# Performance work log

Measured on AMD Instinct MI355X. Metric: run time of the kernel, lower is better.

## Reference

```python
import jax, jax.numpy as jnp
import numpy as np

HEADS = 8
DIM_HEAD = 64
SCALE = DIM_HEAD ** -0.5
THRESH = 0.01


def setup_inputs() -> dict:
    key = jax.random.key(0)
    ks = jax.random.split(key, 5)
    b, n, dim = 4, 2048, 512
    inner = HEADS * DIM_HEAD  # 512
    x = jax.random.normal(ks[0], (b, n, dim), dtype=jnp.float32)
    Wqkv = jax.random.normal(ks[1], (dim, 3 * inner), dtype=jnp.float32) * (dim ** -0.5)
    bqkv = jax.random.normal(ks[2], (3 * inner,), dtype=jnp.float32) * 0.02
    Wout = jax.random.normal(ks[3], (inner, dim), dtype=jnp.float32) * (inner ** -0.5)
    bout = jax.random.normal(ks[4], (dim,), dtype=jnp.float32) * 0.02
    return {"x": x, "Wqkv": Wqkv, "bqkv": bqkv, "Wout": Wout, "bout": bout}


def reference(x, Wqkv, bqkv, Wout, bout):
    b, n, dim = x.shape
    qkv = x @ Wqkv + bqkv  # [b, n, 3*inner]
    q, k, v = jnp.split(qkv, 3, axis=-1)
    # b n (h d) -> b h n d
    split_heads = lambda t: t.reshape(b, n, HEADS, DIM_HEAD).transpose(0, 2, 1, 3)
    q, k, v = split_heads(q), split_heads(k), split_heads(v)
    dots = jnp.einsum('bhid,bhjd->bhij', q, k) * SCALE
    attn = jax.nn.softmax(dots, axis=-1)
    attn = jnp.where(attn > THRESH, attn, jnp.zeros_like(attn))
    out = jnp.einsum('bhij,bhjd->bhid', attn, v)
    out = out.transpose(0, 2, 1, 3).reshape(b, n, HEADS * DIM_HEAD)
    return out @ Wout + bout
```

## Files before the change

### kernel.cpp

```cpp
#include <hip/hip_runtime.h>

#define S_   2048
#define DM   512
#define HD   64
#define BHN  32

typedef unsigned short u16;
typedef __bf16 bf16x8 __attribute__((ext_vector_type(8)));
typedef float  f32x4  __attribute__((ext_vector_type(4)));

__device__ __forceinline__ float bf2f(u16 u) {
    union { unsigned int i; float f; } v; v.i = ((unsigned int)u) << 16; return v.f;
}
__device__ __forceinline__ u16 f2bf(float f) {
    union { float f; unsigned int i; } v; v.f = f;
    unsigned int i = v.i;
    return (u16)((i + 0x7FFFu + ((i >> 16) & 1u)) >> 16);
}
__device__ __forceinline__ void split3(float x, u16& b0, u16& b1, u16& b2) {
    b0 = f2bf(x);
    const float r0 = x - bf2f(b0);
    b1 = f2bf(r0);
    const float r1 = r0 - bf2f(b1);
    b2 = f2bf(r1);
}
__device__ __forceinline__ void split3t(float x, u16& b0, u16& b1, u16& b2) {
    union { float f; unsigned int i; } v; v.f = x;
    const unsigned int i0 = v.i & 0xFFFF0000u;
    b0 = (u16)(i0 >> 16);
    union { float f; unsigned int i; } w0c; w0c.i = i0;
    const float r0 = x - w0c.f;
    union { float f; unsigned int i; } u; u.f = r0;
    const unsigned int i1 = u.i & 0xFFFF0000u;
    b1 = (u16)(i1 >> 16);
    union { float f; unsigned int i; } w1c; w1c.i = i1;
    const float r1 = r0 - w1c.f;
    union { float f; unsigned int i; } z; z.f = r1;
    b2 = (u16)(z.i >> 16);
}

__global__ __launch_bounds__(256) void prep_split_wT(
    const float* __restrict__ W, int N, int total,
    u16* __restrict__ w0, u16* __restrict__ w1, u16* __restrict__ w2)
{
    for (int idx = blockIdx.x * 256 + threadIdx.x; idx < total; idx += gridDim.x * 256) {
        const int n = idx >> 9, k = idx & 511;
        u16 a0, a1, a2;
        split3t(W[(size_t)k * N + n], a0, a1, a2);
        w0[idx] = a0; w1[idx] = a1;
        if (w2) w2[idx] = a2;
    }
}

__global__ __launch_bounds__(256) void gemm_qkv_mfma(
    const float* __restrict__ A, const u16* __restrict__ Wt0, const u16* __restrict__ Wt1,
    const u16* __restrict__ Wt2, const float* __restrict__ bias,
    float* __restrict__ qh, float* __restrict__ kh, u16* __restrict__ khi,
    u16* __restrict__ vt)
{
    __shared__ __attribute__((aligned(16))) u16 As0[128 * 32], As1[128 * 32], As2[128 * 32];
    __shared__ __attribute__((aligned(16))) u16 Bs0[128 * 32], Bs1[128 * 32], Bs2[128 * 32];

    const int t  = threadIdx.x;
    const int m0 = blockIdx.y * 128, n0 = blockIdx.x * 128;
    const int w  = t >> 6, l = t & 63;
    const int wm = (w >> 1) * 64, wn = (w & 1) * 64;
    const int lr = l & 15, lq = l >> 4;

    const f32x4 zero4 = {0.f, 0.f, 0.f, 0.f};
    f32x4 acc[4][4];
#pragma unroll
    for (int i = 0; i < 4; i++)
#pragma unroll
        for (int j = 0; j < 4; j++) acc[i][j] = zero4;

    for (int k0 = 0; k0 < 512; k0 += 32) {
        __syncthreads();
#pragma unroll
        for (int i = 0; i < 4; i++) {
            const int e = t + 256 * i;
            const int r = e >> 3, c4 = (e & 7) * 4;
            const float4 f = *(const float4*)(&A[(size_t)(m0 + r) * 512 + k0 + c4]);
            const float xv[4] = {f.x, f.y, f.z, f.w};
            u16 a0[4], a1[4], a2[4];
#pragma unroll
            for (int j = 0; j < 4; j++) split3t(xv[j], a0[j], a1[j], a2[j]);
            int2 p0, p1, p2;
            p0.x = a0[0] | (a0[1] << 16); p0.y = a0[2] | (a0[3] << 16);
            p1.x = a1[0] | (a1[1] << 16); p1.y = a1[2] | (a1[3] << 16);
            p2.x = a2[0] | (a2[1] << 16); p2.y = a2[2] | (a2[3] << 16);
            *(int2*)(&As0[r * 32 + c4]) = p0;
            *(int2*)(&As1[r * 32 + c4]) = p1;
            *(int2*)(&As2[r * 32 + c4]) = p2;
        }
#pragma unroll
        for (int i = 0; i < 2; i++) {
            const int e = t + 256 * i;
            const int r = e >> 2, c0 = (e & 3) * 8;
            *(int4*)(&Bs0[r * 32 + c0]) = *(const int4*)(&Wt0[(size_t)(n0 + r) * 512 + k0 + c0]);
            *(int4*)(&Bs1[r * 32 + c0]) = *(const int4*)(&Wt1[(size_t)(n0 + r) * 512 + k0 + c0]);
            *(int4*)(&Bs2[r * 32 + c0]) = *(const int4*)(&Wt2[(size_t)(n0 + r) * 512 + k0 + c0]);
        }
        __syncthreads();

#pragma unroll
        for (int i = 0; i < 4; i++) {
            const int ao = (wm + i * 16 + lr) * 32 + lq * 8;
            const bf16x8 a0 = *(const bf16x8*)(&As0[ao]);
            const bf16x8 a1 = *(const bf16x8*)(&As1[ao]);
            const bf16x8 a2 = *(const bf16x8*)(&As2[ao]);
#pragma unroll
            for (int j = 0; j < 4; j++) {
                const int bo = (wn + j * 16 + lr) * 32 + lq * 8;
                const bf16x8 b0 = *(const bf16x8*)(&Bs0[bo]);
                const bf16x8 b1 = *(const bf16x8*)(&Bs1[bo]);
                const bf16x8 b2 = *(const bf16x8*)(&Bs2[bo]);
                f32x4 c = acc[i][j];
                c = __builtin_amdgcn_mfma_f32_16x16x32_bf16(a0, b0, c, 0, 0, 0);
                c = __builtin_amdgcn_mfma_f32_16x16x32_bf16(a0, b1, c, 0, 0, 0);
                c = __builtin_amdgcn_mfma_f32_16x16x32_bf16(a1, b0, c, 0, 0, 0);
                c = __builtin_amdgcn_mfma_f32_16x16x32_bf16(a1, b1, c, 0, 0, 0);
                c = __builtin_amdgcn_mfma_f32_16x16x32_bf16(a0, b2, c, 0, 0, 0);
                c = __builtin_amdgcn_mfma_f32_16x16x32_bf16(a2, b0, c, 0, 0, 0);
                acc[i][j] = c;
            }
        }
    }

#pragma unroll
    for (int j = 0; j < 4; j++) {
        const int n = n0 + wn + j * 16 + lr;
        const float bv = bias[n];
        const int part = n >> 9, within = n & 511;
        const int h = within >> 6, d = within & 63;
#pragma unroll
        for (int i = 0; i < 4; i++) {
#pragma unroll
            for (int r = 0; r < 4; r++) {
                const int m = m0 + wm + i * 16 + lq * 4 + r;
                const int b = m >> 11, ns = m & 2047;
                const float val = acc[i][j][r] + bv;
                if (part == 0) {
                    qh[(((size_t)(b * 8 + h)) * S_ + ns) * HD + d] = val;
                } else if (part == 1) {
                    const size_t kidx = (((size_t)(b * 8 + h)) * S_ + ns) * HD + d;
                    kh[kidx]  = val;
                    khi[kidx] = f2bf(val);
                } else {
                    vt[(((size_t)(b * 8 + h)) * HD + d) * S_ + ns] = f2bf(val);
                }
            }
        }
    }
}

__global__ __launch_bounds__(512) void attn_mfma128(
    const float* __restrict__ q_ws, const float* __restrict__ k_ws,
    const u16* __restrict__ khi_ws, const u16* __restrict__ vt_ws,
    u16* __restrict__ ao_ws)
{
    __shared__ __attribute__((aligned(16))) u16 pool[2][3][4096];
    __shared__ float smaxL[8][32];

    const int t  = threadIdx.x;
    const int w  = t >> 6, l = t & 63;
    const int lr = l & 15, lq = l >> 4;
    const int bh = blockIdx.y, b = bh >> 3, h = bh & 7;
    const int q0 = blockIdx.x * 128;

    const float* qg  = q_ws + ((size_t)bh * S_ + q0) * HD;
    const float* kg0 = k_ws + (size_t)bh * S_ * HD;
    const u16*   kh0 = khi_ws + (size_t)bh * S_ * HD;
    const u16*   vb  = vt_ws + (size_t)bh * HD * S_;

    const int cw = t >> 6, cl = t & 63;
    const int sr = ((cw >> 1) << 4) | (cl & 15);
    const int sd = ((cw & 1) << 5) | (((cl >> 4) & 3) << 3);
    const int sdst = t * 8;

    bf16x8 fq0[2], fq1[2], fq2[2];
#pragma unroll
    for (int h2 = 0; h2 < 2; h2++) {
        __syncthreads();
        {
            const float* src = qg + (size_t)h2 * 4096 + sr * 64 + sd;
            const float4 fA = *(const float4*)(src);
            const float4 fB = *(const float4*)(src + 4);
            const float xv[8] = {fA.x * 0.125f, fA.y * 0.125f, fA.z * 0.125f, fA.w * 0.125f,
                                 fB.x * 0.125f, fB.y * 0.125f, fB.z * 0.125f, fB.w * 0.125f};
            u16 a0[8], a1[8], a2[8];
#pragma unroll
            for (int j = 0; j < 8; j++) split3(xv[j], a0[j], a1[j], a2[j]);
            int4 p0, p1, p2;
            p0.x = a0[0] | (a0[1] << 16); p0.y = a0[2] | (a0[3] << 16);
            p0.z = a0[4] | (a0[5] << 16); p0.w = a0[6] | (a0[7] << 16);
            p1.x = a1[0] | (a1[1] << 16); p1.y = a1[2] | (a1[3] << 16);
            p1.z = a1[4] | (a1[5] << 16); p1.w = a1[6] | (a1[7] << 16);
            p2.x = a2[0] | (a2[1] << 16); p2.y = a2[2] | (a2[3] << 16);
            p2.z = a2[4] | (a2[5] << 16); p2.w = a2[6] | (a2[7] << 16);
            *(int4*)(&pool[0][0][sdst]) = p0;
            *(int4*)(&pool[0][1][sdst]) = p1;
            *(int4*)(&pool[0][2][sdst]) = p2;
        }
        __syncthreads();
        if ((w >> 2) == h2) {
#pragma unroll
            for (int kc = 0; kc < 2; kc++) {
                const int o = ((((w & 3) << 1) + kc) << 9) + l * 8;
                fq0[kc] = *(const bf16x8*)(&pool[0][0][o]);
                fq1[kc] = *(const bf16x8*)(&pool[0][1][o]);
                fq2[kc] = *(const bf16x8*)(&pool[0][2][o]);
            }
        }
    }

    const f32x4 zero4 = {0.f, 0.f, 0.f, 0.f};
    float lsum[4];
#pragma unroll
    for (int r = 0; r < 4; r++) lsum[r] = 0.f;

    int cur = 0;
    {
        const float* src = kg0 + sr * 64 + sd;
        const float4 fA = *(const float4*)(src);
        const float4 fB = *(const float4*)(src + 4);
        __syncthreads();
        const float xv[8] = {fA.x, fA.y, fA.z, fA.w, fB.x, fB.y, fB.z, fB.w};
        u16 a0[8], a1[8], a2[8];
#pragma unroll
        for (int j = 0; j < 8; j++) split3t(xv[j], a0[j], a1[j], a2[j]);
        int4 p0, p1, p2;
        p0.x = a0[0] | (a0[1] << 16); p0.y = a0[2] | (a0[3] << 16);
        p0.z = a0[4] | (a0[5] << 16); p0.w = a0[6] | (a0[7] << 16);
        p1.x = a1[0] | (a1[1] << 16); p1.y = a1[2] | (a1[3] << 16);
        p1.z = a1[4] | (a1[5] << 16); p1.w = a1[6] | (a1[7] << 16);
        p2.x = a2[0] | (a2[1] << 16); p2.y = a2[2] | (a2[3] << 16);
        p2.z = a2[4] | (a2[5] << 16); p2.w = a2[6] | (a2[7] << 16);
        *(int4*)(&pool[0][0][sdst]) = p0;
        *(int4*)(&pool[0][1][sdst]) = p1;
        *(int4*)(&pool[0][2][sdst]) = p2;
        __syncthreads();
    }

    for (int jt = 0; jt < 32; jt++) {
        const int jn = (jt + 1 < 32) ? jt + 1 : 31;
        const float* src = kg0 + (size_t)jn * 4096 + sr * 64 + sd;
        const float4 fA = *(const float4*)(src);
        const float4 fB = *(const float4*)(src + 4);

        const u16* K0c = pool[cur][0];
        const u16* K1c = pool[cur][1];
        const u16* K2c = pool[cur][2];
        float tmax = -1e30f;
#pragma unroll
        for (int nt = 0; nt < 4; nt++) {
            f32x4 aHH = zero4, aC = zero4;
#pragma unroll
            for (int kc = 0; kc < 2; kc++) {
                const int ko = (((nt << 1) + kc) << 9) + l * 8;
                const bf16x8 k0 = *(const bf16x8*)(&K0c[ko]);
                const bf16x8 k1 = *(const bf16x8*)(&K1c[ko]);
                const bf16x8 k2 = *(const bf16x8*)(&K2c[ko]);
                aHH = __builtin_amdgcn_mfma_f32_16x16x32_bf16(fq0[kc], k0, aHH, 0, 0, 0);
                aC  = __builtin_amdgcn_mfma_f32_16x16x32_bf16(fq0[kc], k1, aC, 0, 0, 0);
                aC  = __builtin_amdgcn_mfma_f32_16x16x32_bf16(fq1[kc], k0, aC, 0, 0, 0);
                aC  = __builtin_amdgcn_mfma_f32_16x16x32_bf16(fq1[kc], k1, aC, 0, 0, 0);
                aC  = __builtin_amdgcn_mfma_f32_16x16x32_bf16(fq0[kc], k2, aC, 0, 0, 0);
                aC  = __builtin_amdgcn_mfma_f32_16x16x32_bf16(fq2[kc], k0, aC, 0, 0, 0);
            }
#pragma unroll
            for (int r = 0; r < 4; r++) {
                const float s = fminf(fmaxf(aHH[r] + aC[r], -30.f), 30.f);
                tmax = fmaxf(tmax, s);
                lsum[r] += __expf(s);
            }
        }
#pragma unroll
        for (int off = 1; off < 64; off <<= 1)
            tmax = fmaxf(tmax, __shfl_xor(tmax, off, 64));
        if (l == 0) smaxL[w][jt] = tmax;

        {
            const float xv[8] = {fA.x, fA.y, fA.z, fA.w, fB.x, fB.y, fB.z, fB.w};
            u16 a0[8], a1[8], a2[8];
#pragma unroll
            for (int j = 0; j < 8; j++) split3t(xv[j], a0[j], a1[j], a2[j]);
            int4 p0, p1, p2;
            p0.x = a0[0] | (a0[1] << 16); p0.y = a0[2] | (a0[3] << 16);
            p0.z = a0[4] | (a0[5] << 16); p0.w = a0[6] | (a0[7] << 16);
            p1.x = a1[0] | (a1[1] << 16); p1.y = a1[2] | (a1[3] << 16);
            p1.z = a1[4] | (a1[5] << 16); p1.w = a1[6] | (a1[7] << 16);
            p2.x = a2[0] | (a2[1] << 16); p2.y = a2[2] | (a2[3] << 16);
            p2.z = a2[4] | (a2[5] << 16); p2.w = a2[6] | (a2[7] << 16);
            *(int4*)(&pool[cur ^ 1][0][sdst]) = p0;
            *(int4*)(&pool[cur ^ 1][1][sdst]) = p1;
            *(int4*)(&pool[cur ^ 1][2][sdst]) = p2;
        }
        __syncthreads();
        cur ^= 1;
    }

#pragma unroll
    for (int r = 0; r < 4; r++) {
#pragma unroll
        for (int off = 1; off < 16; off <<= 1)
            lsum[r] += __shfl_xor(lsum[r], off, 64);
    }
    double l_d[4]; float inv_l[4];
#pragma unroll
    for (int r = 0; r < 4; r++) {
        l_d[r] = (double)lsum[r];
        inv_l[r] = 1.0f / lsum[r];
    }

    float zmin4 = fminf(fminf(lsum[0], lsum[1]), fminf(lsum[2], lsum[3]));
    zmin4 = fminf(zmin4, __shfl_xor(zmin4, 16, 64));
    zmin4 = fminf(zmin4, __shfl_xor(zmin4, 32, 64));
    const float sthr = logf(0.0085f * zmin4);

    f32x4 oacc[4];
#pragma unroll
    for (int dt = 0; dt < 4; dt++) oacc[dt] = zero4;

    const int rB = t >> 3, cB = (t & 7) * 8;
    const int chB8 = (((rB >> 4) * 2 + (cB >> 5)) * 64 + (((cB >> 3) & 3) << 4) + (rB & 15)) * 8;
    u16* const Pw = &pool[w >> 2][2][(w & 3) * 1024];

    {
        const int4 kb0 = *(const int4*)(&kh0[(size_t)rB * HD + cB]);
        const int4 vr0 = *(const int4*)(&vb[(size_t)rB * S_ + cB]);
        *(int4*)(&pool[0][0][chB8]) = kb0;
        *(int4*)(&pool[0][1][chB8]) = vr0;
        __syncthreads();
    }
    cur = 0;

    for (int jt = 0; jt < 32; jt++) {
        const int jn = (jt + 1 < 32) ? jt + 1 : 31;
        const int4 kb = *(const int4*)(&kh0[(size_t)jn * 4096 + (size_t)rB * HD + cB]);
        const int4 vr = *(const int4*)(&vb[(size_t)rB * S_ + jn * 64 + cB]);

        const bool live = (smaxL[w][jt] >= sthr);

        if (live) {
            const u16* Kc = pool[cur][0];
#pragma unroll
            for (int nt = 0; nt < 4; nt++) {
                f32x4 sacc = zero4;
#pragma unroll
                for (int kc = 0; kc < 2; kc++) {
                    const bf16x8 k0 = *(const bf16x8*)(&Kc[(((nt << 1) + kc) << 9) + l * 8]);
                    sacc = __builtin_amdgcn_mfma_f32_16x16x32_bf16(fq0[kc], k0, sacc, 0, 0, 0);
                }
#pragma unroll
                for (int r = 0; r < 4; r++) {
                    const float s = fminf(fmaxf(sacc[r], -30.f), 30.f);
                    const float p = __expf(s) * inv_l[r];
                    u16 pb;
                    if (p > 0.0115f) {
                        pb = f2bf(p);
                    } else if (p < 0.009f) {
                        pb = 0;
                    } else {
                        const int row = q0 + w * 16 + lq * 4 + r;
                        const int col = jt * 64 + nt * 16 + lr;
                        const float* qr  = q_ws + ((size_t)bh * S_ + row) * HD;
                        const float* kcv = k_ws + ((size_t)bh * S_ + col) * HD;
                        double s64 = 0.0;
                        for (int d = 0; d < HD; d++) s64 += (double)qr[d] * (double)kcv[d];
                        s64 = fmin(fmax(s64 * 0.125, -30.0), 30.0);
                        const double pd = exp(s64) / l_d[r];
                        pb = (pd > 0.01) ? f2bf((float)pd) : (u16)0;
                    }
                    const int key = nt * 16 + lr;
                    const int pAddr = (((key >> 5) << 6) + (((key >> 3) & 3) << 4) + (lq * 4 + r)) * 8
                                    + (key & 7);
                    Pw[pAddr] = pb;
                }
            }
        }
        *(int4*)(&pool[cur ^ 1][0][chB8]) = kb;
        *(int4*)(&pool[cur ^ 1][1][chB8]) = vr;
        __syncthreads();
        if (live) {
            const u16* Vc = pool[cur][1];
#pragma unroll
            for (int kc = 0; kc < 2; kc++) {
                const bf16x8 ap = *(const bf16x8*)(&Pw[(kc << 9) + l * 8]);
#pragma unroll
                for (int dt = 0; dt < 4; dt++) {
                    const bf16x8 bv = *(const bf16x8*)(&Vc[(((dt << 1) + kc) << 9) + l * 8]);
                    oacc[dt] = __builtin_amdgcn_mfma_f32_16x16x32_bf16(ap, bv, oacc[dt], 0, 0, 0);
                }
            }
        }
        __syncthreads();
        cur ^= 1;
    }

#pragma unroll
    for (int dt = 0; dt < 4; dt++) {
#pragma unroll
        for (int r = 0; r < 4; r++) {
            const int row = q0 + w * 16 + lq * 4 + r;
            const int d   = dt * 16 + lr;
            ao_ws[((size_t)b * S_ + row) * DM + h * HD + d] = f2bf(oacc[dt][r]);
        }
    }
}

__global__ __launch_bounds__(256) void gemm_out_mfma(
    const u16* __restrict__ A, const u16* __restrict__ Wt0, const u16* __restrict__ Wt1,
    const float* __restrict__ bias, float* __restrict__ out)
{
    __shared__ __attribute__((aligned(16))) u16 As[128 * 32];
    __shared__ __attribute__((aligned(16))) u16 Bs0[128 * 32], Bs1[128 * 32];

    const int t  = threadIdx.x;
    const int m0 = blockIdx.y * 128, n0 = blockIdx.x * 128;
    const int w  = t >> 6, l = t & 63;
    const int wm = (w >> 1) * 64, wn = (w & 1) * 64;
    const int lr = l & 15, lq = l >> 4;

    const f32x4 zero4 = {0.f, 0.f, 0.f, 0.f};
    f32x4 acc[4][4];
#pragma unroll
    for (int i = 0; i < 4; i++)
#pragma unroll
        for (int j = 0; j < 4; j++) acc[i][j] = zero4;

    for (int k0 = 0; k0 < 512; k0 += 32) {
        __syncthreads();
#pragma unroll
        for (int i = 0; i < 2; i++) {
            const int e = t + 256 * i;
            const int r = e >> 2, c0 = (e & 3) * 8;
            *(int4*)(&As[r * 32 + c0])  = *(const int4*)(&A  [(size_t)(m0 + r) * 512 + k0 + c0]);
            *(int4*)(&Bs0[r * 32 + c0]) = *(const int4*)(&Wt0[(size_t)(n0 + r) * 512 + k0 + c0]);
            *(int4*)(&Bs1[r * 32 + c0]) = *(const int4*)(&Wt1[(size_t)(n0 + r) * 512 + k0 + c0]);
        }
        __syncthreads();

#pragma unroll
        for (int i = 0; i < 4; i++) {
            const bf16x8 a = *(const bf16x8*)(&As[(wm + i * 16 + lr) * 32 + lq * 8]);
#pragma unroll
            for (int j = 0; j < 4; j++) {
                const int bo = (wn + j * 16 + lr) * 32 + lq * 8;
                const bf16x8 b0 = *(const bf16x8*)(&Bs0[bo]);
                const bf16x8 b1 = *(const bf16x8*)(&Bs1[bo]);
                f32x4 c = acc[i][j];
                c = __builtin_amdgcn_mfma_f32_16x16x32_bf16(a, b0, c, 0, 0, 0);
                c = __builtin_amdgcn_mfma_f32_16x16x32_bf16(a, b1, c, 0, 0, 0);
                acc[i][j] = c;
            }
        }
    }

#pragma unroll
    for (int j = 0; j < 4; j++) {
        const int n = n0 + wn + j * 16 + lr;
        const float bv = bias[n];
#pragma unroll
        for (int i = 0; i < 4; i++) {
#pragma unroll
            for (int r = 0; r < 4; r++) {
                const int m = m0 + wm + i * 16 + lq * 4 + r;
                out[(size_t)m * 512 + n] = acc[i][j][r] + bv;
            }
        }
    }
}

extern "C" void kernel_launch(void* const* d_in, const int* in_sizes, int n_in,
                              void* d_out, int out_size, void* d_ws, size_t ws_size,
                              hipStream_t stream) {
    const float* x = nullptr; const float* Wqkv = nullptr; const float* bqkv = nullptr;
    const float* Wout = nullptr; const float* bout = nullptr;
    for (int i = 0; i < n_in; i++) {
        switch (in_sizes[i]) {
            case 4194304: x    = (const float*)d_in[i]; break;
            case 786432:  Wqkv = (const float*)d_in[i]; break;
            case 1536:    bqkv = (const float*)d_in[i]; break;
            case 262144:  Wout = (const float*)d_in[i]; break;
            case 512:     bout = (const float*)d_in[i]; break;
            default: break;
        }
    }
    if (!x)    x    = (const float*)d_in[0];
    if (!Wqkv) Wqkv = (const float*)d_in[1];
    if (!bqkv) bqkv = (const float*)d_in[2];
    if (!Wout) Wout = (const float*)d_in[3];
    if (!bout) bout = (const float*)d_in[4];

    float* out = (float*)d_out;

    char* ws = (char*)d_ws;
    float* q_ws  = (float*)(ws);
    float* k_ws  = (float*)(ws + (16ull << 20));
    u16* vt_ws = (u16*)(ws + (32ull << 20));
    u16* ao_ws = (u16*)(ws + (40ull << 20));
    u16* khi_ws = (u16*)d_out;
    u16* wt0 = (u16*)(ws + (40ull << 20));
    u16* wt1 = (u16*)(ws + (40ull << 20) + 1572864);
    u16* wt2 = (u16*)(ws + (40ull << 20) + 3145728);
    u16* wo0 = (u16*)(ws + (32ull << 20));
    u16* wo1 = (u16*)(ws + (32ull << 20) + 524288);

    prep_split_wT<<<3072, 256, 0, stream>>>(Wqkv, 1536, 1536 * 512, wt0, wt1, wt2);
    gemm_qkv_mfma<<<dim3(12, 64), 256, 0, stream>>>(
        x, wt0, wt1, wt2, bqkv, q_ws, k_ws, khi_ws, vt_ws);
    attn_mfma128<<<dim3(16, BHN), 512, 0, stream>>>(q_ws, k_ws, khi_ws, vt_ws, ao_ws);
    prep_split_wT<<<1024, 256, 0, stream>>>(Wout, 512, 512 * 512, wo0, wo1, nullptr);
    gemm_out_mfma<<<dim3(4, 64), 256, 0, stream>>>(ao_ws, wo0, wo1, bout, out);
}
```

Baseline: 410.5 us.

## Drop shared-memory K/V staging; read K/V tiles directly from global per wave

Removes the cooperative double-buffered LDS staging of K and V tiles and the two block-wide barriers per key tile, letting each wave read its K and V fragments straight from global memory (likely L2-resident) and skip dead tiles with a per-wave continue. The P tile written to LDS gains an XOR swizzle to reduce bank conflicts, and wave-local lgkmcnt waits replace __syncthreads. This removes barrier stalls and lets sparse waves skip work independently. In exchange it adds redundant global loads across waves and less coalesced accesses, especially the strided V reads.

```diff
diff --git a/kernel.cpp b/kernel.cpp
--- a/kernel.cpp
+++ b/kernel.cpp
@@ -322,80 +322,62 @@
 #pragma unroll
     for (int dt = 0; dt < 4; dt++) oacc[dt] = zero4;
 
-    const int rB = t >> 3, cB = (t & 7) * 8;
-    const int chB8 = (((rB >> 4) * 2 + (cB >> 5)) * 64 + (((cB >> 3) & 3) << 4) + (rB & 15)) * 8;
     u16* const Pw = &pool[w >> 2][2][(w & 3) * 1024];
 
-    {
-        const int4 kb0 = *(const int4*)(&kh0[(size_t)rB * HD + cB]);
-        const int4 vr0 = *(const int4*)(&vb[(size_t)rB * S_ + cB]);
-        *(int4*)(&pool[0][0][chB8]) = kb0;
-        *(int4*)(&pool[0][1][chB8]) = vr0;
-        __syncthreads();
-    }
-    cur = 0;
-
     for (int jt = 0; jt < 32; jt++) {
-        const int jn = (jt + 1 < 32) ? jt + 1 : 31;
-        const int4 kb = *(const int4*)(&kh0[(size_t)jn * 4096 + (size_t)rB * HD + cB]);
-        const int4 vr = *(const int4*)(&vb[(size_t)rB * S_ + jn * 64 + cB]);
-
-        const bool live = (smaxL[w][jt] >= sthr);
-
-        if (live) {
-            const u16* Kc = pool[cur][0];
-#pragma unroll
-            for (int nt = 0; nt < 4; nt++) {
-                f32x4 sacc = zero4;
-#pragma unroll
-                for (int kc = 0; kc < 2; kc++) {
-                    const bf16x8 k0 = *(const bf16x8*)(&Kc[(((nt << 1) + kc) << 9) + l * 8]);
-                    sacc = __builtin_amdgcn_mfma_f32_16x16x32_bf16(fq0[kc], k0, sacc, 0, 0, 0);
+        if (smaxL[w][jt] < sthr) continue;
+
+        const u16* kt = kh0 + (size_t)jt * 4096;
+#pragma unroll
+        for (int nt = 0; nt < 4; nt++) {
+            f32x4 sacc = zero4;
+#pragma unroll
+            for (int kc = 0; kc < 2; kc++) {
+                const bf16x8 k0 = *(const bf16x8*)(&kt[(size_t)(nt * 16 + lr) * HD + kc * 32 + lq * 8]);
+                sacc = __builtin_amdgcn_mfma_f32_16x16x32_bf16(fq0[kc], k0, sacc, 0, 0, 0);
+            }
+#pragma unroll
+            for (int r = 0; r < 4; r++) {
+                const float s = fminf(fmaxf(sacc[r], -30.f), 30.f);
+                const float p = __expf(s) * inv_l[r];
+                u16 pb;
+                if (p > 0.0115f) {
+                    pb = f2bf(p);
+                } else if (p < 0.009f) {
+                    pb = 0;
+                } else {
+                    const int row = q0 + w * 16 + lq * 4 + r;
+                    const int col = jt * 64 + nt * 16 + lr;
+                    const float* qr  = q_ws + ((size_t)bh * S_ + row) * HD;
+                    const float* kcv = k_ws + ((size_t)bh * S_ + col) * HD;
+                    double s64 = 0.0;
+                    for (int d = 0; d < HD; d++) s64 += (double)qr[d] * (double)kcv[d];
+                    s64 = fmin(fmax(s64 * 0.125, -30.0), 30.0);
+                    const double pd = exp(s64) / l_d[r];
+                    pb = (pd > 0.01) ? f2bf((float)pd) : (u16)0;
                 }
-#pragma unroll
-                for (int r = 0; r < 4; r++) {
-                    const float s = fminf(fmaxf(sacc[r], -30.f), 30.f);
-                    const float p = __expf(s) * inv_l[r];
-                    u16 pb;
-                    if (p > 0.0115f) {
-                        pb = f2bf(p);
-                    } else if (p < 0.009f) {
-                        pb = 0;
-                    } else {
-                        const int row = q0 + w * 16 + lq * 4 + r;
-                        const int col = jt * 64 + nt * 16 + lr;
-                        const float* qr  = q_ws + ((size_t)bh * S_ + row) * HD;
-                        const float* kcv = k_ws + ((size_t)bh * S_ + col) * HD;
-                        double s64 = 0.0;
-                        for (int d = 0; d < HD; d++) s64 += (double)qr[d] * (double)kcv[d];
-                        s64 = fmin(fmax(s64 * 0.125, -30.0), 30.0);
-                        const double pd = exp(s64) / l_d[r];
-                        pb = (pd > 0.01) ? f2bf((float)pd) : (u16)0;
-                    }
-                    const int key = nt * 16 + lr;
-                    const int pAddr = (((key >> 5) << 6) + (((key >> 3) & 3) << 4) + (lq * 4 + r)) * 8
-                                    + (key & 7);
-                    Pw[pAddr] = pb;
-                }
-            }
-        }
-        *(int4*)(&pool[cur ^ 1][0][chB8]) = kb;
-        *(int4*)(&pool[cur ^ 1][1][chB8]) = vr;
-        __syncthreads();
-        if (live) {
-            const u16* Vc = pool[cur][1];
-#pragma unroll
-            for (int kc = 0; kc < 2; kc++) {
-                const bf16x8 ap = *(const bf16x8*)(&Pw[(kc << 9) + l * 8]);
-#pragma unroll
-                for (int dt = 0; dt < 4; dt++) {
-                    const bf16x8 bv = *(const bf16x8*)(&Vc[(((dt << 1) + kc) << 9) + l * 8]);
-                    oacc[dt] = __builtin_amdgcn_mfma_f32_16x16x32_bf16(ap, bv, oacc[dt], 0, 0, 0);
-                }
-            }
-        }
-        __syncthreads();
-        cur ^= 1;
+                const int key = nt * 16 + lr;
+                int c = ((key >> 5) << 6) + (((key >> 3) & 3) << 4) + (lq * 4 + r);
+                c ^= (c >> 2) & 7;
+                Pw[c * 8 + (key & 7)] = pb;
+            }
+        }
+        asm volatile("s_waitcnt lgkmcnt(0)" ::: "memory");
+        __builtin_amdgcn_sched_barrier(0);
+
+#pragma unroll
+        for (int kc = 0; kc < 2; kc++) {
+            int cr = (kc << 6) + l;
+            cr ^= (cr >> 2) & 7;
+            const bf16x8 ap = *(const bf16x8*)(&Pw[cr * 8]);
+#pragma unroll
+            for (int dt = 0; dt < 4; dt++) {
+                const bf16x8 bv = *(const bf16x8*)(&vb[(size_t)(dt * 16 + lr) * S_ + jt * 64 + kc * 32 + lq * 8]);
+                oacc[dt] = __builtin_amdgcn_mfma_f32_16x16x32_bf16(ap, bv, oacc[dt], 0, 0, 0);
+            }
+        }
+        asm volatile("s_waitcnt lgkmcnt(0)" ::: "memory");
+        __builtin_amdgcn_sched_barrier(0);
     }
 
 #pragma unroll
```

Measured after the change: 512.8 us. +24.9%, slower.
